# Optimization experiments

Measured on AMD Instinct MI355X. Metric: run time of the kernel, lower is better.

## Reference

```python
import jax, jax.numpy as jnp
import numpy as np

B = 131072
DIM = 64
D_IN = 32
D_OUT = 32
HIDDEN = 512
N_BINS = 8
TAIL = 3.0


def setup_inputs() -> dict:
    key = jax.random.key(0)
    ks = jax.random.split(key, 7)
    x = jax.random.normal(ks[0], (B, DIM), dtype=jnp.float32)
    out_dim = D_OUT * (3 * N_BINS - 1)  # 32 * 23 = 736
    W1 = jax.random.normal(ks[1], (D_IN, HIDDEN), dtype=jnp.float32) / np.sqrt(D_IN)
    b1 = jnp.zeros((HIDDEN,), dtype=jnp.float32)
    W2 = jax.random.normal(ks[2], (HIDDEN, HIDDEN), dtype=jnp.float32) / np.sqrt(HIDDEN)
    b2 = jnp.zeros((HIDDEN,), dtype=jnp.float32)
    W3 = jax.random.normal(ks[3], (HIDDEN, out_dim), dtype=jnp.float32) / np.sqrt(HIDDEN)
    b3 = jnp.zeros((out_dim,), dtype=jnp.float32)
    return {"x": x, "W1": W1, "b1": b1, "W2": W2, "b2": b2, "W3": W3, "b3": b3}


def _gather(t, idx):
    # t: (..., K), idx: (...) -> (...,)
    return jnp.take_along_axis(t, idx[..., None], axis=-1)[..., 0]


def rq_spline_forward(x, widths, heights, derivatives, tail_bound=TAIL):
    K = widths.shape[-1]
    widths = jax.nn.softmax(widths, axis=-1) * 2 * tail_bound
    heights = jax.nn.softmax(heights, axis=-1) * 2 * tail_bound
    derivatives = jax.nn.softplus(derivatives)
    ones = jnp.ones_like(derivatives[..., :1])
    derivatives = jnp.concatenate([ones, derivatives, ones], axis=-1)  # (..., K+1)
    cumwidths = jnp.cumsum(widths, axis=-1)
    cumwidths = jnp.pad(cumwidths, [(0, 0)] * (cumwidths.ndim - 1) + [(1, 0)]) - tail_bound
    cumheights = jnp.cumsum(heights, axis=-1)
    cumheights = jnp.pad(cumheights, [(0, 0)] * (cumheights.ndim - 1) + [(1, 0)]) - tail_bound

    inside = (x >= -tail_bound) & (x <= tail_bound)
    xc = jnp.clip(x, -tail_bound + 1e-6, tail_bound - 1e-6)
    # searchsorted (left): number of knots strictly less than xc
    bin_idx = jnp.sum(cumwidths[..., 1:] < xc[..., None], axis=-1)
    bin_idx = jnp.clip(bin_idx, 0, K - 1)

    w_k = _gather(widths, bin_idx)
    h_k = _gather(heights, bin_idx)
    d_k = _gather(derivatives, bin_idx)
    d_k1 = _gather(derivatives[..., 1:], bin_idx)
    cw_k = _gather(cumwidths, bin_idx)
    ch_k = _gather(cumheights, bin_idx)

    xi = jnp.clip((xc - cw_k) / w_k, 1e-6, 1 - 1e-6)
    s_k = h_k / w_k
    num = h_k * (s_k * xi**2 + d_k * xi * (1 - xi))
    den = s_k + (d_k + d_k1 - 2 * s_k) * xi * (1 - xi)
    y_inside = ch_k + num / den
    log_det_inside = (
        jnp.log(s_k**2 * (d_k1 * xi**2 + 2 * s_k * xi * (1 - xi) + d_k * (1 - xi) ** 2) + 1e-8)
        - jnp.log(den**2 + 1e-8)
    )
    y = jnp.where(inside, y_inside, x)
    log_det = jnp.where(inside, log_det_inside, jnp.zeros_like(x))
    return y, log_det


def reference(x, W1, b1, W2, b2, W3, b3):
    # mask: first D_IN dims conditioned on, last D_OUT transformed
    x_masked = x[:, :D_IN]
    x_transform = x[:, D_IN:]
    h = jax.nn.relu(x_masked @ W1 + b1)
    h = jax.nn.relu(h @ W2 + b2)
    raw = h @ W3 + b3
    raw = raw.reshape(x.shape[0], D_OUT, 3 * N_BINS - 1)
    widths = raw[..., :N_BINS]
    heights = raw[..., N_BINS:2 * N_BINS]
    derivs = raw[..., 2 * N_BINS:]
    y_t, log_det = rq_spline_forward(x_transform, widths, heights, derivs, TAIL)
    y = jnp.concatenate([x_masked, y_t], axis=-1)
    return y, jnp.sum(log_det, axis=-1)
```

## Files before the change

kernel.cpp:

```cpp
#include <hip/hip_runtime.h>
#include <hip/hip_bf16.h>
#include <stdint.h>

typedef __bf16 bf16_t;
typedef _Float16 f16_t;
typedef _Float16 f16x8 __attribute__((ext_vector_type(8)));
typedef float f32x4 __attribute__((ext_vector_type(4)));

#define HID 512
#define NRAW 736
#define NRAW_PAD 768
#define TAILB 3.0f

__device__ __forceinline__ void glds16(const void* g, void* s) {
  __builtin_amdgcn_global_load_lds(
      (const __attribute__((address_space(1))) void*)g,
      (__attribute__((address_space(3))) void*)s, 16, 0, 0);
}
__device__ __forceinline__ float frcp(float x) { return __builtin_amdgcn_rcpf(x); }

__global__ void detect_dtype(const void* x, int* flag) {
  __shared__ int s;
  if (threadIdx.x == 0) s = 0;
  __syncthreads();
  const bf16_t* xb = (const bf16_t*)x;
  int cnt = 0;
  for (int j = 0; j < 16; j++) {
    float v = (float)xb[threadIdx.x * 16 + j];
    if (!(v == v) || fabsf(v) > 64.0f) cnt++;
  }
  atomicAdd(&s, cnt);
  __syncthreads();
  if (threadIdx.x == 0) *flag = (s > 64) ? 1 : 0;
}

__global__ void conv_wb(const void* W1, const void* W2, const void* W3,
                        const void* b1, const void* b2, const void* b3,
                        f16_t* __restrict__ w1t, f16_t* __restrict__ w2t,
                        f16_t* __restrict__ w3t,
                        float* __restrict__ bf1, float* __restrict__ bf2,
                        float* __restrict__ bf3, const int* flagp) {
  const int flag = *flagp;
  auto rd = [&](const void* p, size_t idx) -> float {
    return flag ? ((const float*)p)[idx] : (float)((const bf16_t*)p)[idx];
  };
  int i = blockIdx.x * 256 + threadIdx.x;
  if (i < 512 * 32)  { w1t[i] = (f16_t)rd(W1, (size_t)(i & 31) * 512 + (i >> 5)); return; }
  i -= 512 * 32;
  if (i < 512 * 512) { w2t[i] = (f16_t)rd(W2, (size_t)(i & 511) * 512 + (i >> 9)); return; }
  i -= 512 * 512;
  if (i < NRAW_PAD * 512) {
    int n = i >> 9, k = i & 511;
    int ch = n / 24, e = n % 24;
    w3t[i] = (e < 23) ? (f16_t)rd(W3, (size_t)k * NRAW + ch * 23 + e) : (f16_t)0.0f;
    return;
  }
  i -= NRAW_PAD * 512;
  if (i < 512) { bf1[i] = rd(b1, i); return; }
  i -= 512;
  if (i < 512) { bf2[i] = rd(b2, i); return; }
  i -= 512;
  if (i < NRAW_PAD) {
    int ch = i / 24, e = i % 24;
    bf3[i] = (e < 23) ? rd(b3, (size_t)ch * 23 + e) : 0.0f;
  }
}

__global__ void convert_x(const void* x, f16_t* __restrict__ xf,
                          void* __restrict__ outv, const int* flagp, int n) {
  const int flag = *flagp;
  const int i0 = (blockIdx.x * 256 + threadIdx.x) * 8;
  if (i0 >= n) return;
  const int row = i0 >> 5, col = i0 & 31;
  #pragma unroll
  for (int j = 0; j < 8; j++) {
    const size_t src = (size_t)row * 64 + col + j;
    float v = flag ? ((const float*)x)[src] : (float)((const bf16_t*)x)[src];
    xf[i0 + j] = (f16_t)v;
    if (flag) ((float*)outv)[src] = v;
    else      ((bf16_t*)outv)[src] = (bf16_t)v;
  }
}

__global__ void ld_finalize(const float* __restrict__ ldp, void* __restrict__ outv,
                            const int* __restrict__ flagp, int M) {
  const int i = blockIdx.x * 256 + threadIdx.x;
  if (i >= M) return;
  float s = 0.f;
  #pragma unroll
  for (int n = 0; n < 8; n++) s += ldp[(size_t)n * M + i];
  if (*flagp) ((float*)outv)[(size_t)M * 64 + i] = s;
  else        ((bf16_t*)outv)[(size_t)M * 64 + i] = (bf16_t)s;
}

__launch_bounds__(256)
__global__ void gemm12(const f16_t* __restrict__ X, const f16_t* __restrict__ W1t,
                       const float* __restrict__ b1, const f16_t* __restrict__ W2t,
                       const float* __restrict__ b2, f16_t* __restrict__ H2) {
  constexpr int BK = 64;
  __shared__ __align__(16) f16_t As[128 * BK], Bs[128 * BK];
  const int t = threadIdx.x;
  const int id = blockIdx.x;
  const int xcd = id & 7, s = id >> 3;
  const int n0 = (s & 3) * 128;
  const int m0 = ((s >> 2) * 8 + xcd) * 128;
  const int lrow = t >> 3, lcb = t & 7;
  const int lane = t & 63, w = t >> 6;
  const int wr = (w >> 1) * 64, wc = (w & 1) * 64, wc2 = (w & 1) * 32;
  const int lm = lane & 15, quad = lane >> 4;

  const f16_t* gb[4];
  f16_t* ldb[4];
  #pragma unroll
  for (int r = 0; r < 4; r++) {
    const int row = r * 32 + lrow;
    const int gc = (lcb ^ (row & 7)) * 8;
    gb[r] = W2t + (size_t)(n0 + row) * 512 + gc;
    ldb[r] = &Bs[row * BK + lcb * 8];
  }
  const f16x8* ap[4][2];
  const f16x8* bp[4][2];
  #pragma unroll
  for (int i = 0; i < 4; i++) {
    const int ra = wr + i * 16 + lm, rb = wc + i * 16 + lm;
    #pragma unroll
    for (int ksi = 0; ksi < 2; ksi++) {
      const int qb = ksi * 4 + quad;
      ap[i][ksi] = (const f16x8*)&As[ra * BK + ((qb ^ (ra & 7)) << 3)];
      bp[i][ksi] = (const f16x8*)&Bs[rb * BK + ((qb ^ (rb & 7)) << 3)];
    }
  }
  f16x8 xfr[4];
  #pragma unroll
  for (int i = 0; i < 4; i++)
    xfr[i] = *(const f16x8*)(X + (size_t)(m0 + wr + i * 16 + lm) * 32 + quad * 8);
  const f16_t* w1b0 = W1t + (size_t)(wc2 + lm) * 32 + quad * 8;
  const f16_t* w1b1 = W1t + (size_t)(wc2 + 16 + lm) * 32 + quad * 8;
  const float* b1b0 = b1 + wc2 + lm;
  const float* b1b1 = b1 + wc2 + 16 + lm;
  const int cb0 = (wc2 + lm) >> 3, lw = lm & 7;
  int rbase[4], xt0[4], xt1[4];
  #pragma unroll
  for (int r = 0; r < 4; r++) {
    const int rr = quad * 4 + r;
    rbase[r] = wr * 64 + rr * 64 + lw;
    const int rm = rr & 7;
    xt0[r] = (cb0 ^ rm) << 3;
    xt1[r] = ((cb0 + 2) ^ rm) << 3;
  }

  f32x4 acc[4][4] = {};

  #pragma unroll
  for (int k0i = 0; k0i < 8; k0i++) {
    const int k0 = k0i * 64;
    #pragma unroll
    for (int r = 0; r < 4; r++) glds16(gb[r] + k0, ldb[r]);
    f16x8 w1f0 = *(const f16x8*)(w1b0 + (size_t)k0 * 32);
    f16x8 w1f1 = *(const f16x8*)(w1b1 + (size_t)k0 * 32);
    const float bv0 = b1b0[k0], bv1 = b1b1[k0];
    f32x4 h0[4], h1[4];
    #pragma unroll
    for (int i = 0; i < 4; i++) {
      f32x4 z = {};
      h0[i] = __builtin_amdgcn_mfma_f32_16x16x32_f16(xfr[i], w1f0, z, 0, 0, 0);
      h1[i] = __builtin_amdgcn_mfma_f32_16x16x32_f16(xfr[i], w1f1, z, 0, 0, 0);
    }
    __syncthreads();
    #pragma unroll
    for (int i = 0; i < 4; i++)
      #pragma unroll
      for (int r = 0; r < 4; r++) {
        As[rbase[r] + i * 1024 + xt0[r]] = (f16_t)fmaxf(h0[i][r] + bv0, 0.0f);
        As[rbase[r] + i * 1024 + xt1[r]] = (f16_t)fmaxf(h1[i][r] + bv1, 0.0f);
      }
    __syncthreads();
    #pragma unroll
    for (int ksi = 0; ksi < 2; ksi++) {
      f16x8 af[4], bf[4];
      #pragma unroll
      for (int i = 0; i < 4; i++) af[i] = *ap[i][ksi];
      #pragma unroll
      for (int j = 0; j < 4; j++) bf[j] = *bp[j][ksi];
      #pragma unroll
      for (int i = 0; i < 4; i++)
        #pragma unroll
        for (int j = 0; j < 4; j++)
          acc[i][j] = __builtin_amdgcn_mfma_f32_16x16x32_f16(af[i], bf[j], acc[i][j], 0, 0, 0);
    }
    __syncthreads();
  }
  #pragma unroll
  for (int i = 0; i < 4; i++)
    #pragma unroll
    for (int j = 0; j < 4; j++) {
      const int col = n0 + wc + j * 16 + lm;
      const float bv = b2[col];
      #pragma unroll
      for (int r = 0; r < 4; r++) {
        const int rowi = m0 + wr + i * 16 + quad * 4 + r;
        H2[(size_t)rowi * HID + col] = (f16_t)fmaxf(acc[i][j][r] + bv, 0.0f);
      }
    }
}

#define RSH 104
#define SP1 0.5413248546f

__launch_bounds__(256)
__global__ void gemm3_spline(const f16_t* __restrict__ A, const f16_t* __restrict__ Bt,
                             const float* __restrict__ bias,
                             const void* __restrict__ xorig,
                             void* __restrict__ outv, float* __restrict__ ldp,
                             int M, int r0, const int* __restrict__ flagp) {
  constexpr int BK = 64;
  __shared__ __align__(16) char smem[16384 + 12288];
  f16_t* As = (f16_t*)smem;
  f16_t* Bs = (f16_t*)(smem + 16384);
  f16_t* rawh = (f16_t*)smem;

  const int t = threadIdx.x;
  const int id = blockIdx.x;
  const int xcd = id & 7, s = id >> 3;
  const int ntile = s & 7;
  const int m0 = ((s >> 3) * 8 + xcd) * 128;
  const int n0 = ntile * 96;
  const int lrow = t >> 3, lcb = t & 7;
  const int lane = t & 63, w = t >> 6;
  const int wr = (w >> 1) * 64, wc = (w & 1) * 48;
  const int lm = lane & 15, quad = lane >> 4;
  const int flag = *flagp;

  const int prow = t >> 2, pch = ntile * 4 + (t & 3);
  float xt_pre[2];
  #pragma unroll
  for (int e = 0; e < 2; e++) {
    const size_t gi = (size_t)(r0 + m0 + e * 64 + prow) * 64 + 32 + pch;
    xt_pre[e] = flag ? ((const float*)xorig)[gi] : (float)((const bf16_t*)xorig)[gi];
  }

  const f16_t* ga[4];
  const f16_t* gb[3];
  f16_t* lda[4];
  f16_t* ldb[3];
  #pragma unroll
  for (int r = 0; r < 4; r++) {
    const int row = r * 32 + lrow;
    const int gc = (lcb ^ (row & 7)) * 8;
    ga[r] = A + (size_t)(m0 + row) * 512 + gc;
    lda[r] = &As[row * BK + lcb * 8];
  }
  #pragma unroll
  for (int r = 0; r < 3; r++) {
    const int row = r * 32 + lrow;
    const int gc = (lcb ^ (row & 7)) * 8;
    gb[r] = Bt + (size_t)(n0 + row) * 512 + gc;
    ldb[r] = &Bs[row * BK + lcb * 8];
  }
  const f16x8* ap[4][2];
  const f16x8* bp[3][2];
  #pragma unroll
  for (int ksi = 0; ksi < 2; ksi++) {
    const int qb = ksi * 4 + quad;
    #pragma unroll
    for (int i = 0; i < 4; i++) {
      const int ra = wr + i * 16 + lm;
      ap[i][ksi] = (const f16x8*)&As[ra * BK + ((qb ^ (ra & 7)) << 3)];
    }
    #pragma unroll
    for (int j = 0; j < 3; j++) {
      const int rb = wc + j * 16 + lm;
      bp[j][ksi] = (const f16x8*)&Bs[rb * BK + ((qb ^ (rb & 7)) << 3)];
    }
  }

  f32x4 acc[4][3] = {};

  #pragma unroll
  for (int k0 = 0; k0 < 512; k0 += BK) {
    #pragma unroll
    for (int r = 0; r < 4; r++) glds16(ga[r] + k0, lda[r]);
    #pragma unroll
    for (int r = 0; r < 3; r++) glds16(gb[r] + k0, ldb[r]);
    __syncthreads();
    #pragma unroll
    for (int ksi = 0; ksi < 2; ksi++) {
      f16x8 af[4], bf[3];
      #pragma unroll
      for (int i = 0; i < 4; i++) af[i] = *ap[i][ksi];
      #pragma unroll
      for (int j = 0; j < 3; j++) bf[j] = *bp[j][ksi];
      #pragma unroll
      for (int i = 0; i < 4; i++)
        #pragma unroll
        for (int j = 0; j < 3; j++)
          acc[i][j] = __builtin_amdgcn_mfma_f32_16x16x32_f16(af[i], bf[j], acc[i][j], 0, 0, 0);
    }
    __syncthreads();
  }

  #pragma unroll
  for (int i = 0; i < 4; i++)
    #pragma unroll
    for (int j = 0; j < 3; j++) {
      const int col = wc + j * 16 + lm;
      const float bv = bias[n0 + col];
      #pragma unroll
      for (int r = 0; r < 4; r++)
        rawh[(wr + i * 16 + quad * 4 + r) * RSH + col] = (f16_t)(acc[i][j][r] + bv);
    }
  __syncthreads();

  #pragma unroll
  for (int e = 0; e < 2; e++) {
    const int row = e * 64 + prow;
    const f16_t* c16 = &rawh[row * RSH + (t & 3) * 24];
    const f16x8 v0 = *(const f16x8*)(c16);
    const f16x8 v1 = *(const f16x8*)(c16 + 8);
    const f16x8 v2 = *(const f16x8*)(c16 + 16);
    float wa[8], ha[8], da[7];
    #pragma unroll
    for (int j = 0; j < 8; j++) { wa[j] = (float)v0[j]; ha[j] = (float)v1[j]; }
    #pragma unroll
    for (int j = 0; j < 7; j++) da[j] = (float)v2[j];

    const float xt = xt_pre[e];
    const bool inside = (xt >= -TAILB) && (xt <= TAILB);
    const float xc = fminf(fmaxf(xt, -TAILB + 1e-6f), TAILB - 1e-6f);

    float mw = wa[0], mh = ha[0];
    #pragma unroll
    for (int j = 1; j < 8; j++) { mw = fmaxf(mw, wa[j]); mh = fmaxf(mh, ha[j]); }
    float ew[8], eh[8], sew = 0.f, seh = 0.f;
    #pragma unroll
    for (int j = 0; j < 8; j++) {
      ew[j] = __expf(wa[j] - mw); sew += ew[j];
      eh[j] = __expf(ha[j] - mh); seh += eh[j];
    }
    const float wsc = 6.0f * frcp(sew), hsc = 6.0f * frcp(seh);
    #pragma unroll
    for (int j = 0; j < 8; j++) { ew[j] *= wsc; eh[j] *= hsc; }

    float accw = -TAILB, runh = -TAILB;
    float cwk = -TAILB, chk = -TAILB;
    float wk = ew[0], hk = eh[0];
    float dkr = SP1, dk1r = da[0];
    #pragma unroll
    for (int i = 0; i < 7; i++) {
      accw += ew[i];
      runh += eh[i];
      const bool cond = accw < xc;
      cwk  = cond ? accw : cwk;
      chk  = cond ? runh : chk;
      wk   = cond ? ew[i + 1] : wk;
      hk   = cond ? eh[i + 1] : hk;
      dkr  = cond ? da[i] : dkr;
      dk1r = cond ? ((i == 6) ? SP1 : da[i + 1]) : dk1r;
    }
    const float dk  = fmaxf(dkr, 0.0f)  + __logf(1.0f + __expf(-fabsf(dkr)));
    const float dk1 = fmaxf(dk1r, 0.0f) + __logf(1.0f + __expf(-fabsf(dk1r)));

    const float rwk = frcp(wk);
    float xi = (xc - cwk) * rwk;
    xi = fminf(fmaxf(xi, 1e-6f), 1.0f - 1e-6f);
    const float om = 1.0f - xi;
    const float sl = hk * rwk;
    const float num = hk * (sl * xi * xi + dk * xi * om);
    const float den = sl + (dk + dk1 - 2.0f * sl) * xi * om;
    const float y_in = chk + num * frcp(den);
    const float t1 = sl * sl * (dk1 * xi * xi + 2.0f * sl * xi * om + dk * om * om);
    const float ld_in = __logf(t1 + 1e-8f) - __logf(den * den + 1e-8f);

    const float yv = inside ? y_in : xt;
    const float ldv = inside ? ld_in : 0.0f;

    const size_t grow = (size_t)(r0 + m0 + row);
    if (flag) ((float*)outv)[grow * 64 + 32 + pch] = yv;
    else      ((bf16_t*)outv)[grow * 64 + 32 + pch] = (bf16_t)yv;

    float l = ldv + __shfl_down(ldv, 1, 4);
    l += __shfl_down(l, 2, 4);
    if ((t & 3) == 0) ldp[(size_t)ntile * M + grow] = l;
  }
}

extern "C" void kernel_launch(void* const* d_in, const int* in_sizes, int n_in,
                              void* d_out, int out_size, void* d_ws, size_t ws_size,
                              hipStream_t stream) {
  const void* x  = d_in[0];
  const void* W1 = d_in[1];
  const void* b1 = d_in[2];
  const void* W2 = d_in[3];
  const void* b2 = d_in[4];
  const void* W3 = d_in[5];
  const void* b3 = d_in[6];
  const int M = in_sizes[0] / 64;

  char* ws = (char*)d_ws;
  size_t off = 0;
  auto alloc = [&](size_t bytes) {
    void* p = ws + off;
    off += (bytes + 255) & ~(size_t)255;
    return p;
  };
  int*   flag = (int*)alloc(256);
  float* bf1  = (float*)alloc(512 * 4);
  float* bf2  = (float*)alloc(512 * 4);
  float* bf3  = (float*)alloc(NRAW_PAD * 4);
  f16_t* W1t  = (f16_t*)alloc((size_t)512 * 32 * 2);
  f16_t* W2t  = (f16_t*)alloc((size_t)512 * 512 * 2);
  f16_t* W3t  = (f16_t*)alloc((size_t)NRAW_PAD * 512 * 2);
  f16_t* xf   = (f16_t*)alloc((size_t)M * 32 * 2);
  float* ldp  = (float*)alloc((size_t)8 * M * 4);

  const size_t per_row = (size_t)HID * 2;
  size_t avail = (ws_size > off + 4096) ? (ws_size - off - 4096) : 0;
  long rows = (long)(avail / per_row);
  rows -= rows % 1024;
  if (rows > M) rows = M;
  if (rows < 1024) rows = 1024;

  f16_t* h2 = (f16_t*)alloc((size_t)rows * HID * 2);

  detect_dtype<<<1, 256, 0, stream>>>(x, flag);
  conv_wb<<<2631, 256, 0, stream>>>(W1, W2, W3, b1, b2, b3,
                                    W1t, W2t, W3t, bf1, bf2, bf3, flag);
  convert_x<<<(M * 32 / 8 + 255) / 256, 256, 0, stream>>>(x, xf, d_out, flag, M * 32);

  for (int r0 = 0; r0 < M; r0 += (int)rows) {
    const int mc = (int)((M - r0 < rows) ? (M - r0) : rows);
    const int mt = mc / 128;
    gemm12<<<mt * 4, 256, 0, stream>>>(
        xf + (size_t)r0 * 32, W1t, bf1, W2t, bf2, h2);
    gemm3_spline<<<mt * 8, 256, 0, stream>>>(
        h2, W3t, bf3, x, d_out, ldp, M, r0, flag);
  }
  ld_finalize<<<(M + 255) / 256, 256, 0, stream>>>(ldp, d_out, flag, M);
}
```

Baseline: 368.9 us.

## Fuse x fp16 conversion into gemm12 and vectorize layer-1 LDS stores

Drops the separate fp16 copy of x: gemm12 now reads the original input (fp32 or bf16) and converts it in registers, while convert_x only copies the passthrough half to the output with vector loads and stores. The layer-1 MFMA operands are swapped so each lane holds four consecutive hidden columns, which lets the ReLU outputs go to LDS as 4-wide stores with float4 bias loads. W1 fragments are prefetched one iteration ahead and the trailing barrier is skipped on the last iteration. These cut a global round trip and reduce scalar LDS store traffic, at the cost of redundant x conversion across the four N-tile blocks.

```diff
diff --git a/kernel.cpp b/kernel.cpp
--- a/kernel.cpp
+++ b/kernel.cpp
@@ -5,6 +5,7 @@
 typedef __bf16 bf16_t;
 typedef _Float16 f16_t;
 typedef _Float16 f16x8 __attribute__((ext_vector_type(8)));
+typedef _Float16 f16x4 __attribute__((ext_vector_type(4)));
 typedef float f32x4 __attribute__((ext_vector_type(4)));
 
 #define HID 512
@@ -66,19 +67,19 @@
   }
 }
 
-__global__ void convert_x(const void* x, f16_t* __restrict__ xf,
-                          void* __restrict__ outv, const int* flagp, int n) {
+__global__ void convert_x(const void* x, void* __restrict__ outv,
+                          const int* flagp, int n) {
   const int flag = *flagp;
   const int i0 = (blockIdx.x * 256 + threadIdx.x) * 8;
   if (i0 >= n) return;
   const int row = i0 >> 5, col = i0 & 31;
-  #pragma unroll
-  for (int j = 0; j < 8; j++) {
-    const size_t src = (size_t)row * 64 + col + j;
-    float v = flag ? ((const float*)x)[src] : (float)((const bf16_t*)x)[src];
-    xf[i0 + j] = (f16_t)v;
-    if (flag) ((float*)outv)[src] = v;
-    else      ((bf16_t*)outv)[src] = (bf16_t)v;
+  const size_t src = (size_t)row * 64 + col;
+  if (flag) {
+    const float4* s4 = (const float4*)((const float*)x + src);
+    float4* d4 = (float4*)((float*)outv + src);
+    d4[0] = s4[0]; d4[1] = s4[1];
+  } else {
+    *(uint4*)((bf16_t*)outv + src) = *(const uint4*)((const bf16_t*)x + src);
   }
 }
 
@@ -94,9 +95,10 @@
 }
 
 __launch_bounds__(256)
-__global__ void gemm12(const f16_t* __restrict__ X, const f16_t* __restrict__ W1t,
+__global__ void gemm12(const void* __restrict__ xorig, const f16_t* __restrict__ W1t,
                        const float* __restrict__ b1, const f16_t* __restrict__ W2t,
-                       const float* __restrict__ b2, f16_t* __restrict__ H2) {
+                       const float* __restrict__ b2, f16_t* __restrict__ H2,
+                       int r0, const int* __restrict__ flagp) {
   constexpr int BK = 64;
   __shared__ __align__(16) f16_t As[128 * BK], Bs[128 * BK];
   const int t = threadIdx.x;
@@ -108,6 +110,7 @@
   const int lane = t & 63, w = t >> 6;
   const int wr = (w >> 1) * 64, wc = (w & 1) * 64, wc2 = (w & 1) * 32;
   const int lm = lane & 15, quad = lane >> 4;
+  const int flag = *flagp;
 
   const f16_t* gb[4];
   f16_t* ldb[4];
@@ -132,48 +135,76 @@
   }
   f16x8 xfr[4];
   #pragma unroll
-  for (int i = 0; i < 4; i++)
-    xfr[i] = *(const f16x8*)(X + (size_t)(m0 + wr + i * 16 + lm) * 32 + quad * 8);
-  const f16_t* w1b0 = W1t + (size_t)(wc2 + lm) * 32 + quad * 8;
-  const f16_t* w1b1 = W1t + (size_t)(wc2 + 16 + lm) * 32 + quad * 8;
-  const float* b1b0 = b1 + wc2 + lm;
-  const float* b1b1 = b1 + wc2 + 16 + lm;
-  const int cb0 = (wc2 + lm) >> 3, lw = lm & 7;
-  int rbase[4], xt0[4], xt1[4];
-  #pragma unroll
-  for (int r = 0; r < 4; r++) {
-    const int rr = quad * 4 + r;
-    rbase[r] = wr * 64 + rr * 64 + lw;
-    const int rm = rr & 7;
-    xt0[r] = (cb0 ^ rm) << 3;
-    xt1[r] = ((cb0 + 2) ^ rm) << 3;
+  for (int i = 0; i < 4; i++) {
+    const size_t xrow = (size_t)(r0 + m0 + wr + i * 16 + lm);
+    if (flag) {
+      const float* px = (const float*)xorig + xrow * 64 + quad * 8;
+      const float4 a = *(const float4*)px;
+      const float4 b = *(const float4*)(px + 4);
+      f16x8 v;
+      v[0] = (f16_t)a.x; v[1] = (f16_t)a.y; v[2] = (f16_t)a.z; v[3] = (f16_t)a.w;
+      v[4] = (f16_t)b.x; v[5] = (f16_t)b.y; v[6] = (f16_t)b.z; v[7] = (f16_t)b.w;
+      xfr[i] = v;
+    } else {
+      const bf16_t* px = (const bf16_t*)xorig + xrow * 64 + quad * 8;
+      f16x8 v;
+      #pragma unroll
+      for (int j = 0; j < 8; j++) v[j] = (f16_t)(float)px[j];
+      xfr[i] = v;
+    }
+  }
+  const f16_t* w1p0 = W1t + (size_t)(wc2 + lm) * 32 + quad * 8;
+  const f16_t* w1p1 = W1t + (size_t)(wc2 + 16 + lm) * 32 + quad * 8;
+  const float* b1p0 = b1 + wc2 + 4 * quad;
+  const float* b1p1 = b1 + wc2 + 16 + 4 * quad;
+  f16_t* wadr[4][2];
+  #pragma unroll
+  for (int i = 0; i < 4; i++) {
+    const int row = wr + i * 16 + lm;
+    #pragma unroll
+    for (int Tl = 0; Tl < 2; Tl++) {
+      const int cb = (wc2 >> 3) + 2 * Tl + (quad >> 1);
+      wadr[i][Tl] = &As[row * BK + ((cb ^ (row & 7)) << 3) + 4 * (quad & 1)];
+    }
   }
 
   f32x4 acc[4][4] = {};
+  f16x8 w1f0 = *(const f16x8*)w1p0;
+  f16x8 w1f1 = *(const f16x8*)w1p1;
 
   #pragma unroll
   for (int k0i = 0; k0i < 8; k0i++) {
     const int k0 = k0i * 64;
     #pragma unroll
     for (int r = 0; r < 4; r++) glds16(gb[r] + k0, ldb[r]);
-    f16x8 w1f0 = *(const f16x8*)(w1b0 + (size_t)k0 * 32);
-    f16x8 w1f1 = *(const f16x8*)(w1b1 + (size_t)k0 * 32);
-    const float bv0 = b1b0[k0], bv1 = b1b1[k0];
-    f32x4 h0[4], h1[4];
+    const float4 bv0 = *(const float4*)(b1p0 + k0);
+    const float4 bv1 = *(const float4*)(b1p1 + k0);
+    f32x4 h[4][2];
     #pragma unroll
     for (int i = 0; i < 4; i++) {
       f32x4 z = {};
-      h0[i] = __builtin_amdgcn_mfma_f32_16x16x32_f16(xfr[i], w1f0, z, 0, 0, 0);
-      h1[i] = __builtin_amdgcn_mfma_f32_16x16x32_f16(xfr[i], w1f1, z, 0, 0, 0);
+      h[i][0] = __builtin_amdgcn_mfma_f32_16x16x32_f16(w1f0, xfr[i], z, 0, 0, 0);
+      h[i][1] = __builtin_amdgcn_mfma_f32_16x16x32_f16(w1f1, xfr[i], z, 0, 0, 0);
+    }
+    if (k0i < 7) {
+      w1f0 = *(const f16x8*)(w1p0 + (size_t)(k0 + 64) * 32);
+      w1f1 = *(const f16x8*)(w1p1 + (size_t)(k0 + 64) * 32);
     }
     __syncthreads();
     #pragma unroll
-    for (int i = 0; i < 4; i++)
-      #pragma unroll
-      for (int r = 0; r < 4; r++) {
-        As[rbase[r] + i * 1024 + xt0[r]] = (f16_t)fmaxf(h0[i][r] + bv0, 0.0f);
-        As[rbase[r] + i * 1024 + xt1[r]] = (f16_t)fmaxf(h1[i][r] + bv1, 0.0f);
-      }
+    for (int i = 0; i < 4; i++) {
+      f16x4 v0, v1;
+      v0[0] = (f16_t)fmaxf(h[i][0][0] + bv0.x, 0.0f);
+      v0[1] = (f16_t)fmaxf(h[i][0][1] + bv0.y, 0.0f);
+      v0[2] = (f16_t)fmaxf(h[i][0][2] + bv0.z, 0.0f);
+      v0[3] = (f16_t)fmaxf(h[i][0][3] + bv0.w, 0.0f);
+      v1[0] = (f16_t)fmaxf(h[i][1][0] + bv1.x, 0.0f);
+      v1[1] = (f16_t)fmaxf(h[i][1][1] + bv1.y, 0.0f);
+      v1[2] = (f16_t)fmaxf(h[i][1][2] + bv1.z, 0.0f);
+      v1[3] = (f16_t)fmaxf(h[i][1][3] + bv1.w, 0.0f);
+      *(f16x4*)wadr[i][0] = v0;
+      *(f16x4*)wadr[i][1] = v1;
+    }
     __syncthreads();
     #pragma unroll
     for (int ksi = 0; ksi < 2; ksi++) {
@@ -188,7 +219,7 @@
         for (int j = 0; j < 4; j++)
           acc[i][j] = __builtin_amdgcn_mfma_f32_16x16x32_f16(af[i], bf[j], acc[i][j], 0, 0, 0);
     }
-    __syncthreads();
+    if (k0i < 7) __syncthreads();
   }
   #pragma unroll
   for (int i = 0; i < 4; i++)
@@ -410,7 +441,6 @@
   f16_t* W1t  = (f16_t*)alloc((size_t)512 * 32 * 2);
   f16_t* W2t  = (f16_t*)alloc((size_t)512 * 512 * 2);
   f16_t* W3t  = (f16_t*)alloc((size_t)NRAW_PAD * 512 * 2);
-  f16_t* xf   = (f16_t*)alloc((size_t)M * 32 * 2);
   float* ldp  = (float*)alloc((size_t)8 * M * 4);
 
   const size_t per_row = (size_t)HID * 2;
@@ -425,13 +455,12 @@
   detect_dtype<<<1, 256, 0, stream>>>(x, flag);
   conv_wb<<<2631, 256, 0, stream>>>(W1, W2, W3, b1, b2, b3,
                                     W1t, W2t, W3t, bf1, bf2, bf3, flag);
-  convert_x<<<(M * 32 / 8 + 255) / 256, 256, 0, stream>>>(x, xf, d_out, flag, M * 32);
+  convert_x<<<(M * 32 / 8 + 255) / 256, 256, 0, stream>>>(x, d_out, flag, M * 32);
 
   for (int r0 = 0; r0 < M; r0 += (int)rows) {
     const int mc = (int)((M - r0 < rows) ? (M - r0) : rows);
     const int mt = mc / 128;
-    gemm12<<<mt * 4, 256, 0, stream>>>(
-        xf + (size_t)r0 * 32, W1t, bf1, W2t, bf2, h2);
+    gemm12<<<mt * 4, 256, 0, stream>>>(x, W1t, bf1, W2t, bf2, h2, r0, flag);
     gemm3_spline<<<mt * 8, 256, 0, stream>>>(
         h2, W3t, bf3, x, d_out, ldp, M, r0, flag);
   }
```

Result: faster. 340.7 us (-7.7%).
